# Performance work log

Measured on AMD Instinct MI355X. Metric: run time of the kernel, lower is better.

## Reference

```python
import jax, jax.numpy as jnp
import numpy as np

D = 48


def setup_inputs() -> dict:
    key = jax.random.key(0)
    k1, k2, k3, k4, k5 = jax.random.split(key, 5)
    B, N, d = 4, 512, D
    x = jax.random.normal(k1, (B, N, d), dtype=jnp.float32)
    # Linear(2d, 2d) and Linear(2d, d); stored as (in, out) so y = x @ W + b
    s1 = 1.0 / np.sqrt(2 * d)
    W1 = jax.random.uniform(k2, (2 * d, 2 * d), dtype=jnp.float32, minval=-s1, maxval=s1)
    b1 = jax.random.uniform(k3, (2 * d,), dtype=jnp.float32, minval=-s1, maxval=s1)
    W2 = jax.random.uniform(k4, (2 * d, d), dtype=jnp.float32, minval=-s1, maxval=s1)
    b2 = jax.random.uniform(k5, (d,), dtype=jnp.float32, minval=-s1, maxval=s1)
    return {"x": x, "W1": W1, "b1": b1, "W2": W2, "b2": b2}


def reference(x, W1, b1, W2, b2):
    B, N, d = x.shape
    # pairwise concat: [B, N, N, 2d] with (i, j) = (x_i, x_j)
    xi = jnp.broadcast_to(x[:, :, None, :], (B, N, N, d))
    xj = jnp.broadcast_to(x[:, None, :, :], (B, N, N, d))
    cat = jnp.concatenate([xi, xj], axis=-1)
    h = jax.nn.gelu(cat @ W1 + b1, approximate=False)  # torch GELU is exact erf form
    p = h @ W2 + b2  # [B, N, N, d]
    mask = jnp.triu(jnp.ones((N, N), dtype=bool), 1)  # j > i masked
    p = jnp.where(mask[None, :, :, None], 0.0, p)
    w = jnp.sqrt(jnp.sum(p * p, axis=-1))  # frobenius norm over feature dim -> [B, N, N]
    w = jnp.where(mask[None, :, :], -1e9, w)
    w = jax.nn.softmax(w, axis=-1)[..., None]  # softmax over j
    return jnp.sum(w * p, axis=2)  # [B, N, d]
```

## Files before the change

### kernel.cpp

```cpp
#include <hip/hip_runtime.h>
#include <hip/hip_bf16.h>
#include <math.h>

#define DD 48
#define NN 512
#define TWO_D 96
#define ROWS 2048

typedef __attribute__((ext_vector_type(8))) short bf16x8;
typedef __attribute__((ext_vector_type(4))) float f32x4;

__device__ __forceinline__ float gelu_poly(float u) {
    const float uc = fminf(fmaxf(u, -3.5777f), 3.5777f);
    const float v = uc * uc;
    float E = fmaf(v, -1.04448e-6f, 4.61896e-5f);
    E = fmaf(v, E, -8.62284e-4f);
    E = fmaf(v, E, 9.22138e-3f);
    E = fmaf(v, E, -6.58353e-2f);
    E = fmaf(v, E, 3.98855e-1f);
    return u * fmaf(uc, E, 0.5f);
}

__global__ __launch_bounds__(256) void precompute_kernel(
        const float* __restrict__ x,
        const float* __restrict__ W1,
        const float* __restrict__ b1,
        const float* __restrict__ W2,
        float* __restrict__ Aout,
        float* __restrict__ Bout,
        __hip_bfloat16* __restrict__ W2T) {
    if (blockIdx.x == ROWS / 4) {
        for (int idx = threadIdx.x; idx < DD * TWO_D; idx += 256) {
            const int f = idx / TWO_D;
            const int k = idx - f * TWO_D;
            W2T[idx] = __float2bfloat16(W2[k * DD + f]);
        }
        return;
    }
    const int wave = threadIdx.x >> 6;
    const int lane = threadIdx.x & 63;
    const int row = blockIdx.x * 4 + wave;
    __shared__ float xs[4][DD];
    if (threadIdx.x < 4 * DD)
        xs[threadIdx.x / DD][threadIdx.x % DD] = x[blockIdx.x * 4 * DD + threadIdx.x];
    __syncthreads();
    for (int t = lane; t < TWO_D; t += 64) {
        float a0 = 0.f, a1 = 0.f;
#pragma unroll 8
        for (int k = 0; k < DD; ++k) {
            const float xv = xs[wave][k];
            a0 = fmaf(xv, W1[k * TWO_D + t], a0);
            a1 = fmaf(xv, W1[(DD + k) * TWO_D + t], a1);
        }
        Aout[row * TWO_D + t] = a0 + b1[t];
        Bout[row * TWO_D + t] = a1;
    }
}

#define PROCESS_ROW(I_, ROW_, CSTART_, lacc_, oacc_)                              \
  {                                                                               \
    float av[3][8];                                                               \
    _Pragma("unroll")                                                             \
    for (int ks = 0; ks < 3; ++ks) {                                              \
      const float4 a0 = *(const float4*)&Arow[(size_t)(ROW_)*TWO_D + ks*32 + q8]; \
      const float4 a1 = *(const float4*)&Arow[(size_t)(ROW_)*TWO_D + ks*32 + q8 + 4]; \
      av[ks][0]=a0.x; av[ks][1]=a0.y; av[ks][2]=a0.z; av[ks][3]=a0.w;             \
      av[ks][4]=a1.x; av[ks][5]=a1.y; av[ks][6]=a1.z; av[ks][7]=a1.w;             \
    }                                                                             \
    const int nch = ((I_) + 16) >> 4;                                             \
    const float* __restrict__ Bj = Bbase + (size_t)(((CSTART_) << 4) + n) * TWO_D;\
    float4 pb[6];                                                                 \
    if ((CSTART_) < nch) {                                                        \
      _Pragma("unroll")                                                           \
      for (int ks = 0; ks < 3; ++ks) {                                            \
        pb[2*ks]   = *(const float4*)&Bj[ks*32 + q8];                             \
        pb[2*ks+1] = *(const float4*)&Bj[ks*32 + q8 + 4];                         \
      }                                                                           \
    }                                                                             \
    for (int c = (CSTART_); c < nch; c += 4) {                                    \
      const int j0 = c << 4;                                                      \
      const bool hn = (c + 4) < nch;                                              \
      const float* __restrict__ Bjn = Bj + (ptrdiff_t)(64 * TWO_D);               \
      f32x4 acc[3] = {{0.f,0.f,0.f,0.f},{0.f,0.f,0.f,0.f},{0.f,0.f,0.f,0.f}};     \
      _Pragma("unroll")                                                           \
      for (int ks = 0; ks < 3; ++ks) {                                            \
        const float4 bv0 = pb[2*ks];                                              \
        const float4 bv1 = pb[2*ks+1];                                            \
        if (hn) {                                                                 \
          pb[2*ks]   = *(const float4*)&Bjn[ks*32 + q8];                          \
          pb[2*ks+1] = *(const float4*)&Bjn[ks*32 + q8 + 4];                      \
        }                                                                         \
        float h[8];                                                               \
        h[0] = gelu_poly(av[ks][0] + bv0.x);                                      \
        h[1] = gelu_poly(av[ks][1] + bv0.y);                                      \
        h[2] = gelu_poly(av[ks][2] + bv0.z);                                      \
        h[3] = gelu_poly(av[ks][3] + bv0.w);                                      \
        h[4] = gelu_poly(av[ks][4] + bv1.x);                                      \
        h[5] = gelu_poly(av[ks][5] + bv1.y);                                      \
        h[6] = gelu_poly(av[ks][6] + bv1.z);                                      \
        h[7] = gelu_poly(av[ks][7] + bv1.w);                                      \
        union { bf16x8 v; __hip_bfloat162 h2[4]; } hf;                            \
        _Pragma("unroll")                                                         \
        for (int pp = 0; pp < 4; ++pp)                                            \
          hf.h2[pp] = __float22bfloat162_rn(make_float2(h[2*pp], h[2*pp+1]));     \
        acc[0] = __builtin_amdgcn_mfma_f32_16x16x32_bf16(bfrag[0][ks], hf.v, acc[0], 0, 0, 0); \
        acc[1] = __builtin_amdgcn_mfma_f32_16x16x32_bf16(bfrag[1][ks], hf.v, acc[1], 0, 0, 0); \
        acc[2] = __builtin_amdgcn_mfma_f32_16x16x32_bf16(bfrag[2][ks], hf.v, acc[2], 0, 0, 0); \
      }                                                                           \
      Bj = Bjn;                                                                   \
      float pv[3][4];                                                             \
      float ss = 0.f;                                                             \
      _Pragma("unroll")                                                           \
      for (int t = 0; t < 3; ++t)                                                 \
        _Pragma("unroll")                                                         \
        for (int r = 0; r < 4; ++r) {                                             \
          const float pz = acc[t][r] + b2v[t][r];                                 \
          pv[t][r] = pz;                                                          \
          ss = fmaf(pz, pz, ss);                                                  \
        }                                                                         \
      ss += __shfl_xor(ss, 16);                                                   \
      ss += __shfl_xor(ss, 32);                                                   \
      const int j = j0 + n;                                                       \
      const float ew = (j <= (I_))                                                \
          ? __builtin_amdgcn_exp2f(sqrtf(ss) * 1.44269504f) : 0.f;                \
      lacc_ += ew;                                                                \
      _Pragma("unroll")                                                           \
      for (int t = 0; t < 3; ++t)                                                 \
        _Pragma("unroll")                                                         \
        for (int r = 0; r < 4; ++r)                                               \
          oacc_[t][r] = fmaf(ew, pv[t][r], oacc_[t][r]);                          \
    }                                                                             \
  }

__global__ __launch_bounds__(256) void pair_softmax_kernel(
        const float* __restrict__ Arow,
        const float* __restrict__ Brow,
        const __hip_bfloat16* __restrict__ W2T,
        const float* __restrict__ b2,
        float* __restrict__ out) {
    const int batch = blockIdx.x >> 8;
    const int pr = blockIdx.x & 255;
    const int iH = (NN - 1) - pr;
    const int iL = pr;
    const int cH = (iH >> 4) + 1;
    const int rowH = batch * NN + iH;
    const int rowL = batch * NN + iL;
    const float* __restrict__ Bbase = Brow + (size_t)batch * NN * TWO_D;

    const int tid = threadIdx.x;
    const int wave = tid >> 6;
    const int lane = tid & 63;
    const int n = lane & 15;
    const int q = lane >> 4;
    const int q8 = q * 8;

    bf16x8 bfrag[3][3];
#pragma unroll
    for (int t = 0; t < 3; ++t)
#pragma unroll
        for (int ks = 0; ks < 3; ++ks)
            bfrag[t][ks] = *(const bf16x8*)&W2T[(t * 16 + n) * TWO_D + ks * 32 + q8];
    float b2v[3][4];
#pragma unroll
    for (int t = 0; t < 3; ++t)
#pragma unroll
        for (int r = 0; r < 4; ++r) b2v[t][r] = b2[t * 16 + 4 * q + r];

    float lH = 0.f, lL = 0.f;
    float oH[3][4] = {{0.f,0.f,0.f,0.f},{0.f,0.f,0.f,0.f},{0.f,0.f,0.f,0.f}};
    float oL[3][4] = {{0.f,0.f,0.f,0.f},{0.f,0.f,0.f,0.f},{0.f,0.f,0.f,0.f}};

    PROCESS_ROW(iH, rowH, wave, lH, oH);
    const int cstartL = (wave + 128 - cH) & 3;
    PROCESS_ROW(iL, rowL, cstartL, lL, oL);

#pragma unroll
    for (int d = 1; d <= 8; d <<= 1) {
        lH += __shfl_xor(lH, d);
        lL += __shfl_xor(lL, d);
#pragma unroll
        for (int t = 0; t < 3; ++t)
#pragma unroll
            for (int r = 0; r < 4; ++r) {
                oH[t][r] += __shfl_xor(oH[t][r], d);
                oL[t][r] += __shfl_xor(oL[t][r], d);
            }
    }
    __shared__ float lred[4][2];
    __shared__ float ored[4][2][DD];
    if (n == 0) {
#pragma unroll
        for (int t = 0; t < 3; ++t)
#pragma unroll
            for (int r = 0; r < 4; ++r) {
                ored[wave][0][t * 16 + 4 * q + r] = oH[t][r];
                ored[wave][1][t * 16 + 4 * q + r] = oL[t][r];
            }
    }
    if (lane == 0) { lred[wave][0] = lH; lred[wave][1] = lL; }
    __syncthreads();
    if (tid < 2 * DD) {
        const int sel = tid / DD;
        const int f = tid - sel * DD;
        float L = 0.f, O = 0.f;
#pragma unroll
        for (int wv = 0; wv < 4; ++wv) {
            L += lred[wv][sel];
            O += ored[wv][sel][f];
        }
        const int row = sel ? rowL : rowH;
        out[row * DD + f] = O / L;
    }
}

extern "C" void kernel_launch(void* const* d_in, const int* in_sizes, int n_in,
                              void* d_out, int out_size, void* d_ws, size_t ws_size,
                              hipStream_t stream) {
    const float* x  = (const float*)d_in[0];
    const float* W1 = (const float*)d_in[1];
    const float* b1 = (const float*)d_in[2];
    const float* W2 = (const float*)d_in[3];
    const float* b2 = (const float*)d_in[4];
    float* outp = (float*)d_out;

    float* A  = (float*)d_ws;
    float* Bb = A + ROWS * TWO_D;
    __hip_bfloat16* W2T = (__hip_bfloat16*)(Bb + ROWS * TWO_D);

    precompute_kernel<<<ROWS / 4 + 1, 256, 0, stream>>>(x, W1, b1, W2, A, Bb, W2T);
    pair_softmax_kernel<<<1024, 256, 0, stream>>>(A, Bb, W2T, b2, outp);
}
```

Before: 97.70 us.

## Store B projections as bf16 and process two chunks per loop iteration

The per-column B projection is now written in bf16, which halves the bytes streamed from memory in the pair loop, and is unpacked with shifts and masks. The chunk loop is also unrolled by two, with independent accumulators and double prefetch buffers, so MFMA and GELU work from two chunks can overlap. The cost is a precision loss on B before the GELU and higher register pressure from the second set of buffers and accumulators.

```diff
diff --git a/kernel.cpp b/kernel.cpp
--- a/kernel.cpp
+++ b/kernel.cpp
@@ -9,6 +9,7 @@
 
 typedef __attribute__((ext_vector_type(8))) short bf16x8;
 typedef __attribute__((ext_vector_type(4))) float f32x4;
+typedef __attribute__((ext_vector_type(4))) unsigned int u32x4;
 
 __device__ __forceinline__ float gelu_poly(float u) {
     const float uc = fminf(fmaxf(u, -3.5777f), 3.5777f);
@@ -21,13 +22,16 @@
     return u * fmaf(uc, E, 0.5f);
 }
 
+__device__ __forceinline__ float bflo(unsigned int u) { return __uint_as_float(u << 16); }
+__device__ __forceinline__ float bfhi(unsigned int u) { return __uint_as_float(u & 0xffff0000u); }
+
 __global__ __launch_bounds__(256) void precompute_kernel(
         const float* __restrict__ x,
         const float* __restrict__ W1,
         const float* __restrict__ b1,
         const float* __restrict__ W2,
         float* __restrict__ Aout,
-        float* __restrict__ Bout,
+        __hip_bfloat16* __restrict__ Bout,
         __hip_bfloat16* __restrict__ W2T) {
     if (blockIdx.x == ROWS / 4) {
         for (int idx = threadIdx.x; idx < DD * TWO_D; idx += 256) {
@@ -53,88 +57,101 @@
             a1 = fmaf(xv, W1[(DD + k) * TWO_D + t], a1);
         }
         Aout[row * TWO_D + t] = a0 + b1[t];
-        Bout[row * TWO_D + t] = a1;
-    }
-}
-
-#define PROCESS_ROW(I_, ROW_, CSTART_, lacc_, oacc_)                              \
-  {                                                                               \
-    float av[3][8];                                                               \
-    _Pragma("unroll")                                                             \
-    for (int ks = 0; ks < 3; ++ks) {                                              \
-      const float4 a0 = *(const float4*)&Arow[(size_t)(ROW_)*TWO_D + ks*32 + q8]; \
+        Bout[row * TWO_D + t] = __float2bfloat16(a1);
+    }
+}
+
+
+#define LOAD_PB(PB_, PTR_)                                                      \
+  { _Pragma("unroll")                                                           \
+    for (int ks = 0; ks < 3; ++ks)                                              \
+      PB_[ks] = *(const u32x4*)&(PTR_)[ks * 32 + q8]; }
+
+#define CHUNK_MFMA(PB_, ACC_, PF_, NPTR_)                                       \
+  { _Pragma("unroll")                                                           \
+    for (int ks = 0; ks < 3; ++ks) {                                            \
+      const unsigned int w0 = PB_[ks].x, w1 = PB_[ks].y,                        \
+                         w2 = PB_[ks].z, w3 = PB_[ks].w;                        \
+      if (PF_) PB_[ks] = *(const u32x4*)&(NPTR_)[ks * 32 + q8];                 \
+      float h[8];                                                               \
+      h[0] = gelu_poly(av[ks][0] + bflo(w0));                                   \
+      h[1] = gelu_poly(av[ks][1] + bfhi(w0));                                   \
+      h[2] = gelu_poly(av[ks][2] + bflo(w1));                                   \
+      h[3] = gelu_poly(av[ks][3] + bfhi(w1));                                   \
+      h[4] = gelu_poly(av[ks][4] + bflo(w2));                                   \
+      h[5] = gelu_poly(av[ks][5] + bfhi(w2));                                   \
+      h[6] = gelu_poly(av[ks][6] + bflo(w3));                                   \
+      h[7] = gelu_poly(av[ks][7] + bfhi(w3));                                   \
+      union { bf16x8 v; __hip_bfloat162 h2[4]; } hf;                            \
+      _Pragma("unroll")                                                         \
+      for (int pp = 0; pp < 4; ++pp)                                            \
+        hf.h2[pp] = __float22bfloat162_rn(make_float2(h[2*pp], h[2*pp+1]));     \
+      ACC_[0] = __builtin_amdgcn_mfma_f32_16x16x32_bf16(bfrag[0][ks], hf.v, ACC_[0], 0, 0, 0); \
+      ACC_[1] = __builtin_amdgcn_mfma_f32_16x16x32_bf16(bfrag[1][ks], hf.v, ACC_[1], 0, 0, 0); \
+      ACC_[2] = __builtin_amdgcn_mfma_f32_16x16x32_bf16(bfrag[2][ks], hf.v, ACC_[2], 0, 0, 0); \
+    } }
+
+#define CHUNK_EPI(J0_, I_, ACC_, L_, O_)                                        \
+  { float pv[3][4];                                                             \
+    float ss = 0.f;                                                             \
+    _Pragma("unroll")                                                           \
+    for (int t = 0; t < 3; ++t)                                                 \
+      _Pragma("unroll")                                                         \
+      for (int r = 0; r < 4; ++r) {                                             \
+        const float pz = ACC_[t][r] + b2v[t][r];                                \
+        pv[t][r] = pz;                                                          \
+        ss = fmaf(pz, pz, ss);                                                  \
+      }                                                                         \
+    ss += __shfl_xor(ss, 16);                                                   \
+    ss += __shfl_xor(ss, 32);                                                   \
+    const int j = (J0_) + n;                                                    \
+    const float ew = (j <= (I_))                                                \
+        ? __builtin_amdgcn_exp2f(sqrtf(ss) * 1.44269504f) : 0.f;                \
+    L_ += ew;                                                                   \
+    _Pragma("unroll")                                                           \
+    for (int t = 0; t < 3; ++t)                                                 \
+      _Pragma("unroll")                                                         \
+      for (int r = 0; r < 4; ++r)                                               \
+        O_[t][r] = fmaf(ew, pv[t][r], O_[t][r]); }
+
+#define PROCESS_ROW_DUAL(I_, ROW_, CSTART_, L_, O_)                             \
+  { float av[3][8];                                                             \
+    _Pragma("unroll")                                                           \
+    for (int ks = 0; ks < 3; ++ks) {                                            \
+      const float4 a0 = *(const float4*)&Arow[(size_t)(ROW_)*TWO_D + ks*32 + q8];     \
       const float4 a1 = *(const float4*)&Arow[(size_t)(ROW_)*TWO_D + ks*32 + q8 + 4]; \
-      av[ks][0]=a0.x; av[ks][1]=a0.y; av[ks][2]=a0.z; av[ks][3]=a0.w;             \
-      av[ks][4]=a1.x; av[ks][5]=a1.y; av[ks][6]=a1.z; av[ks][7]=a1.w;             \
-    }                                                                             \
-    const int nch = ((I_) + 16) >> 4;                                             \
-    const float* __restrict__ Bj = Bbase + (size_t)(((CSTART_) << 4) + n) * TWO_D;\
-    float4 pb[6];                                                                 \
-    if ((CSTART_) < nch) {                                                        \
-      _Pragma("unroll")                                                           \
-      for (int ks = 0; ks < 3; ++ks) {                                            \
-        pb[2*ks]   = *(const float4*)&Bj[ks*32 + q8];                             \
-        pb[2*ks+1] = *(const float4*)&Bj[ks*32 + q8 + 4];                         \
-      }                                                                           \
-    }                                                                             \
-    for (int c = (CSTART_); c < nch; c += 4) {                                    \
-      const int j0 = c << 4;                                                      \
-      const bool hn = (c + 4) < nch;                                              \
-      const float* __restrict__ Bjn = Bj + (ptrdiff_t)(64 * TWO_D);               \
-      f32x4 acc[3] = {{0.f,0.f,0.f,0.f},{0.f,0.f,0.f,0.f},{0.f,0.f,0.f,0.f}};     \
-      _Pragma("unroll")                                                           \
-      for (int ks = 0; ks < 3; ++ks) {                                            \
-        const float4 bv0 = pb[2*ks];                                              \
-        const float4 bv1 = pb[2*ks+1];                                            \
-        if (hn) {                                                                 \
-          pb[2*ks]   = *(const float4*)&Bjn[ks*32 + q8];                          \
-          pb[2*ks+1] = *(const float4*)&Bjn[ks*32 + q8 + 4];                      \
-        }                                                                         \
-        float h[8];                                                               \
-        h[0] = gelu_poly(av[ks][0] + bv0.x);                                      \
-        h[1] = gelu_poly(av[ks][1] + bv0.y);                                      \
-        h[2] = gelu_poly(av[ks][2] + bv0.z);                                      \
-        h[3] = gelu_poly(av[ks][3] + bv0.w);                                      \
-        h[4] = gelu_poly(av[ks][4] + bv1.x);                                      \
-        h[5] = gelu_poly(av[ks][5] + bv1.y);                                      \
-        h[6] = gelu_poly(av[ks][6] + bv1.z);                                      \
-        h[7] = gelu_poly(av[ks][7] + bv1.w);                                      \
-        union { bf16x8 v; __hip_bfloat162 h2[4]; } hf;                            \
-        _Pragma("unroll")                                                         \
-        for (int pp = 0; pp < 4; ++pp)                                            \
-          hf.h2[pp] = __float22bfloat162_rn(make_float2(h[2*pp], h[2*pp+1]));     \
-        acc[0] = __builtin_amdgcn_mfma_f32_16x16x32_bf16(bfrag[0][ks], hf.v, acc[0], 0, 0, 0); \
-        acc[1] = __builtin_amdgcn_mfma_f32_16x16x32_bf16(bfrag[1][ks], hf.v, acc[1], 0, 0, 0); \
-        acc[2] = __builtin_amdgcn_mfma_f32_16x16x32_bf16(bfrag[2][ks], hf.v, acc[2], 0, 0, 0); \
-      }                                                                           \
-      Bj = Bjn;                                                                   \
-      float pv[3][4];                                                             \
-      float ss = 0.f;                                                             \
-      _Pragma("unroll")                                                           \
-      for (int t = 0; t < 3; ++t)                                                 \
-        _Pragma("unroll")                                                         \
-        for (int r = 0; r < 4; ++r) {                                             \
-          const float pz = acc[t][r] + b2v[t][r];                                 \
-          pv[t][r] = pz;                                                          \
-          ss = fmaf(pz, pz, ss);                                                  \
-        }                                                                         \
-      ss += __shfl_xor(ss, 16);                                                   \
-      ss += __shfl_xor(ss, 32);                                                   \
-      const int j = j0 + n;                                                       \
-      const float ew = (j <= (I_))                                                \
-          ? __builtin_amdgcn_exp2f(sqrtf(ss) * 1.44269504f) : 0.f;                \
-      lacc_ += ew;                                                                \
-      _Pragma("unroll")                                                           \
-      for (int t = 0; t < 3; ++t)                                                 \
-        _Pragma("unroll")                                                         \
-        for (int r = 0; r < 4; ++r)                                               \
-          oacc_[t][r] = fmaf(ew, pv[t][r], oacc_[t][r]);                          \
-    }                                                                             \
-  }
+      av[ks][0]=a0.x; av[ks][1]=a0.y; av[ks][2]=a0.z; av[ks][3]=a0.w;           \
+      av[ks][4]=a1.x; av[ks][5]=a1.y; av[ks][6]=a1.z; av[ks][7]=a1.w;           \
+    }                                                                           \
+    const int nch = ((I_) + 16) >> 4;                                           \
+    int c = (CSTART_);                                                          \
+    const __hip_bfloat16* __restrict__ Bp =                                     \
+        Bbase + (size_t)((c << 4) + n) * TWO_D;                                 \
+    u32x4 pbA[3], pbB[3];                                                       \
+    if (c < nch) LOAD_PB(pbA, Bp);                                              \
+    if (c + 4 < nch) LOAD_PB(pbB, Bp + 64 * TWO_D);                             \
+    for (; c + 4 < nch; c += 8) {                                               \
+      const bool pfA = (c + 8) < nch;                                           \
+      const bool pfB = (c + 12) < nch;                                          \
+      const __hip_bfloat16* __restrict__ BpA = Bp + 128 * TWO_D;                \
+      const __hip_bfloat16* __restrict__ BpB = Bp + 192 * TWO_D;                \
+      f32x4 accA[3] = {{0.f,0.f,0.f,0.f},{0.f,0.f,0.f,0.f},{0.f,0.f,0.f,0.f}};  \
+      f32x4 accB[3] = {{0.f,0.f,0.f,0.f},{0.f,0.f,0.f,0.f},{0.f,0.f,0.f,0.f}};  \
+      CHUNK_MFMA(pbA, accA, pfA, BpA);                                          \
+      CHUNK_MFMA(pbB, accB, pfB, BpB);                                          \
+      CHUNK_EPI((c << 4), I_, accA, L_, O_);                                    \
+      CHUNK_EPI(((c + 4) << 4), I_, accB, L_, O_);                              \
+      Bp = BpA;                                                                 \
+    }                                                                           \
+    if (c < nch) {                                                              \
+      f32x4 accA[3] = {{0.f,0.f,0.f,0.f},{0.f,0.f,0.f,0.f},{0.f,0.f,0.f,0.f}};  \
+      CHUNK_MFMA(pbA, accA, false, Bp);                                         \
+      CHUNK_EPI((c << 4), I_, accA, L_, O_);                                    \
+    } }
 
 __global__ __launch_bounds__(256) void pair_softmax_kernel(
         const float* __restrict__ Arow,
-        const float* __restrict__ Brow,
+        const __hip_bfloat16* __restrict__ Brow,
         const __hip_bfloat16* __restrict__ W2T,
         const float* __restrict__ b2,
         float* __restrict__ out) {
@@ -145,7 +162,7 @@
     const int cH = (iH >> 4) + 1;
     const int rowH = batch * NN + iH;
     const int rowL = batch * NN + iL;
-    const float* __restrict__ Bbase = Brow + (size_t)batch * NN * TWO_D;
+    const __hip_bfloat16* __restrict__ Bbase = Brow + (size_t)batch * NN * TWO_D;
 
     const int tid = threadIdx.x;
     const int wave = tid >> 6;
@@ -170,9 +187,9 @@
     float oH[3][4] = {{0.f,0.f,0.f,0.f},{0.f,0.f,0.f,0.f},{0.f,0.f,0.f,0.f}};
     float oL[3][4] = {{0.f,0.f,0.f,0.f},{0.f,0.f,0.f,0.f},{0.f,0.f,0.f,0.f}};
 
-    PROCESS_ROW(iH, rowH, wave, lH, oH);
+    PROCESS_ROW_DUAL(iH, rowH, wave, lH, oH);
     const int cstartL = (wave + 128 - cH) & 3;
-    PROCESS_ROW(iL, rowL, cstartL, lL, oL);
+    PROCESS_ROW_DUAL(iL, rowL, cstartL, lL, oL);
 
 #pragma unroll
     for (int d = 1; d <= 8; d <<= 1) {
@@ -223,9 +240,9 @@
     const float* b2 = (const float*)d_in[4];
     float* outp = (float*)d_out;
 
-    float* A  = (float*)d_ws;
-    float* Bb = A + ROWS * TWO_D;
-    __hip_bfloat16* W2T = (__hip_bfloat16*)(Bb + ROWS * TWO_D);
+    float* A = (float*)d_ws;
+    __hip_bfloat16* Bb  = (__hip_bfloat16*)(A + ROWS * TWO_D);
+    __hip_bfloat16* W2T = Bb + ROWS * TWO_D;
 
     precompute_kernel<<<ROWS / 4 + 1, 256, 0, stream>>>(x, W1, b1, W2, A, Bb, W2T);
     pair_softmax_kernel<<<1024, 256, 0, stream>>>(A, Bb, W2T, b2, outp);
```

Result: faster. 92.07 us (-5.8%).
